# Performance work log

Measured on AMD Instinct MI355X. Metric: run time of the kernel, lower is better.

The kernel has to match this reference:

```python
import jax, jax.numpy as jnp
import numpy as np

COST_CLASS, COST_BBOX, COST_MASK = 1.0, 5.0, 2.0
EPS = 1e-6


def setup_inputs() -> dict:
    key = jax.random.key(0)
    k = jax.random.split(key, 8)
    B, Q, M, C1, H, W = 8, 300, 100, 81, 128, 128
    pred_logits = jax.random.normal(k[0], (B, Q, C1), jnp.float32)
    # boxes as valid xyxy in [0,1]: lo in [0,.5], size in [0,.5]
    plo = jax.random.uniform(k[1], (B, Q, 2)) * 0.5
    psz = jax.random.uniform(k[2], (B, Q, 2)) * 0.5
    pred_boxes = jnp.concatenate([plo, plo + psz], axis=-1)
    pred_masks = jax.random.normal(k[3], (B, Q, H, W), jnp.float32)
    gt_labels = jax.random.randint(k[4], (B, M), 0, C1, dtype=jnp.int32)
    glo = jax.random.uniform(k[5], (B, M, 2)) * 0.5
    gsz = jax.random.uniform(k[6], (B, M, 2)) * 0.5
    gt_boxes = jnp.concatenate([glo, glo + gsz], axis=-1)
    gt_masks = (jax.random.uniform(k[7], (B, M, H, W)) > 0.5).astype(jnp.float32)
    valid = jnp.ones((B, M), jnp.bool_)
    return dict(pred_logits=pred_logits, pred_boxes=pred_boxes, pred_masks=pred_masks,
                gt_labels=gt_labels, gt_boxes=gt_boxes, gt_masks=gt_masks, valid=valid)


def _giou(b1, b2):
    # b1 [Q,4], b2 [M,4] (xyxy) -> [Q,M] generalized IoU
    lt = jnp.maximum(b1[:, None, :2], b2[None, :, :2])
    rb = jnp.minimum(b1[:, None, 2:], b2[None, :, 2:])
    wh = jnp.clip(rb - lt, 0.0)
    inter = wh[..., 0] * wh[..., 1]
    a1 = (b1[:, 2] - b1[:, 0]) * (b1[:, 3] - b1[:, 1])
    a2 = (b2[:, 2] - b2[:, 0]) * (b2[:, 3] - b2[:, 1])
    union = a1[:, None] + a2[None, :] - inter
    iou = inter / (union + EPS)
    ltm = jnp.minimum(b1[:, None, :2], b2[None, :, :2])
    rbm = jnp.maximum(b1[:, None, 2:], b2[None, :, 2:])
    whm = jnp.clip(rbm - ltm, 0.0)
    am = whm[..., 0] * whm[..., 1]
    return iou - (am - union) / (am + EPS)


@jax.jit
def _cost_matrix(pred_logits, pred_boxes, pred_masks, gt_labels, gt_boxes, gt_masks):
    B, Q = pred_logits.shape[:2]
    M = gt_labels.shape[1]
    probs = jax.nn.softmax(pred_logits, axis=-1)                      # [B,Q,C+1]
    idx = jnp.broadcast_to(gt_labels[:, None, :].astype(jnp.int32), (B, Q, M))
    cost_class = -jnp.take_along_axis(probs, idx, axis=2)             # [B,Q,M]
    # L1 cdist
    cost_bbox = jnp.abs(pred_boxes[:, :, None, :] - gt_boxes[:, None, :, :]).sum(-1)
    cost_giou = -jax.vmap(_giou)(pred_boxes, gt_boxes)                # [B,Q,M]
    # dice cost
    pm = jax.nn.sigmoid(pred_masks).reshape(B, Q, -1)                 # [B,Q,HW]
    gm = gt_masks.reshape(B, M, -1).astype(pm.dtype)                  # [B,M,HW]
    num = 2.0 * jnp.einsum('bqc,bmc->bqm', pm, gm)
    den = pm.sum(-1)[:, :, None] + gm.sum(-1)[:, None, :]
    cost_mask = 1.0 - num / (den + EPS)
    # NOTE: faithful to source quirk -- giou term is folded into cost_bbox
    # and therefore weighted by COST_BBOX.
    return (COST_CLASS * cost_class + COST_BBOX * (cost_bbox + cost_giou)
            + COST_MASK * cost_mask)


def _hungarian(cost):
    # Jonker-Volgenant style shortest-augmenting-path assignment (e-maxx).
    # cost: np [n,m] with n <= m. Returns p[m]: row assigned to each col (-1 if none).
    n, m = cost.shape
    u = np.zeros(n)
    v = np.zeros(m)
    p = np.full(m, -1, np.int64)
    for i in range(n):
        minv = np.full(m, np.inf)
        way = np.full(m, -1, np.int64)
        used = np.zeros(m, bool)
        cur_row, j0 = i, -1
        while True:
            cur = cost[cur_row] - u[cur_row] - v
            upd = (~used) & (cur < minv)
            minv[upd] = cur[upd]
            way[upd] = j0
            mv = np.where(used, np.inf, minv)
            j1 = int(np.argmin(mv))
            delta = mv[j1]
            u[i] += delta
            uj = np.nonzero(used)[0]
            if uj.size:
                u[p[uj]] += delta
                v[uj] -= delta
            minv[~used] -= delta
            used[j1] = True
            j0 = j1
            cur_row = p[j1]
            if cur_row == -1:
                break
        j = j0
        while j != -1:
            jp = way[j]
            p[j] = p[jp] if jp != -1 else i
            j = jp
    return p


def reference(pred_logits, pred_boxes, pred_masks, gt_labels, gt_boxes, gt_masks, valid):
    # valid is all-ones (num_gt == max_objects for every sample), so the
    # per-sample variable-size slicing in the torch loop reduces to full M.
    C = _cost_matrix(pred_logits, pred_boxes, pred_masks, gt_labels, gt_boxes, gt_masks)
    Cn = np.asarray(C, dtype=np.float64)
    preds, gts = [], []
    for b in range(Cn.shape[0]):
        # solve on transpose: rows = gt (M=100) <= cols = queries (Q=300)
        p = _hungarian(Cn[b].T)            # p[q] = matched gt index or -1
        q = np.nonzero(p >= 0)[0]          # sorted pred indices (scipy convention)
        preds.append(q)
        gts.append(p[q])
    pred_idx = jnp.asarray(np.stack(preds), dtype=jnp.int32)  # [B, M]
    gt_idx = jnp.asarray(np.stack(gts), dtype=jnp.int32)      # [B, M]
    return C, pred_idx, gt_idx
```

## Files before the change

kernel.cpp:

```cpp
#include <hip/hip_runtime.h>

#define HW 16384
#define NQ 300
#define NM 100
#define NB 8
#define NC 81
#define KCH 1024
#define NKC 16
#define CTP 304

typedef __attribute__((ext_vector_type(8))) short frag8;
typedef __attribute__((ext_vector_type(4))) float float4v;
typedef __attribute__((ext_vector_type(4))) unsigned short ushort4v;

__device__ __forceinline__ unsigned short f2bf(float f) {
  union { float f; unsigned u; } c; c.f = f;
  unsigned r = c.u + 0x7FFFu + ((c.u >> 16) & 1u);
  return (unsigned short)(r >> 16);
}

__global__ __launch_bounds__(256) void prep_kernel(
    const float* __restrict__ pmask, const float* __restrict__ gmask,
    unsigned short* __restrict__ pm, unsigned short* __restrict__ gm,
    float* __restrict__ psum, float* __restrict__ gsum) {
  int row = blockIdx.x;
  int t = threadIdx.x;
  bool isP = row < NB * NQ;
  const float* srcf = isP ? (pmask + (size_t)row * HW)
                          : (gmask + (size_t)(row - NB * NQ) * HW);
  unsigned short* dst = isP ? (pm + (size_t)row * HW)
                            : (gm + (size_t)(row - NB * NQ) * HW);
  const float4v* src = (const float4v*)srcf;
  float s = 0.f;
  for (int i = t; i < HW / 4; i += 256) {
    float4v x = src[i];
    float y0, y1, y2, y3;
    if (isP) {
      y0 = 1.f / (1.f + __expf(-x.x));
      y1 = 1.f / (1.f + __expf(-x.y));
      y2 = 1.f / (1.f + __expf(-x.z));
      y3 = 1.f / (1.f + __expf(-x.w));
    } else { y0 = x.x; y1 = x.y; y2 = x.z; y3 = x.w; }
    s += (y0 + y1) + (y2 + y3);
    ushort4v o = { f2bf(y0), f2bf(y1), f2bf(y2), f2bf(y3) };
    *(ushort4v*)(dst + i * 4) = o;
  }
  for (int off = 32; off > 0; off >>= 1) s += __shfl_xor(s, off, 64);
  __shared__ float red[4];
  int wave = t >> 6, lane = t & 63;
  if (lane == 0) red[wave] = s;
  __syncthreads();
  if (t == 0) {
    float tot = (red[0] + red[1]) + (red[2] + red[3]);
    if (isP) psum[row] = tot; else gsum[row - NB * NQ] = tot;
  }
}

__global__ __launch_bounds__(256) void softmax_kernel(
    const float* __restrict__ logits, float* __restrict__ probs) {
  int wave = threadIdx.x >> 6, lane = threadIdx.x & 63;
  int row = blockIdx.x * 4 + wave;
  const float* in = logits + (size_t)row * NC;
  float x0 = (lane < NC) ? in[lane] : -1e30f;
  float x1 = (lane + 64 < NC) ? in[lane + 64] : -1e30f;
  float mx = fmaxf(x0, x1);
  for (int off = 32; off > 0; off >>= 1) mx = fmaxf(mx, __shfl_xor(mx, off, 64));
  float e0 = (lane < NC) ? __expf(x0 - mx) : 0.f;
  float e1 = (lane + 64 < NC) ? __expf(x1 - mx) : 0.f;
  float s = e0 + e1;
  for (int off = 32; off > 0; off >>= 1) s += __shfl_xor(s, off, 64);
  float inv = 1.f / s;
  if (lane < NC) probs[(size_t)row * NC + lane] = e0 * inv;
  if (lane + 64 < NC) probs[(size_t)row * NC + lane + 64] = e1 * inv;
}

__global__ __launch_bounds__(64) void dot_kernel(
    const unsigned short* __restrict__ pm, const unsigned short* __restrict__ gm,
    float* __restrict__ dotv) {
  int qt = blockIdx.x;
  int b = blockIdx.y >> 4, kc = blockIdx.y & 15;
  int lane = threadIdx.x;
  int q0 = qt * 16;
  int row_a = q0 + (lane & 15);
  int ra = (row_a < NQ) ? row_a : NQ - 1;
  int koff = (lane >> 4) * 8;
  const unsigned short* pA = pm + ((size_t)b * NQ + ra) * HW + kc * KCH + koff;
  const unsigned short* pB0 = gm + (size_t)b * NM * HW + kc * KCH + koff;
  const unsigned short* pB[7];
#pragma unroll
  for (int mt = 0; mt < 7; ++mt) {
    int row_b = mt * 16 + (lane & 15);
    int rb = (row_b < NM) ? row_b : NM - 1;
    pB[mt] = pB0 + (size_t)rb * HW;
  }
  float4v acc[7];
#pragma unroll
  for (int mt = 0; mt < 7; ++mt) acc[mt] = (float4v){0.f, 0.f, 0.f, 0.f};
#pragma unroll 2
  for (int k = 0; k < KCH; k += 32) {
    frag8 a = *(const frag8*)(pA + k);
#pragma unroll
    for (int mt = 0; mt < 7; ++mt) {
      frag8 bb = *(const frag8*)(pB[mt] + k);
      acc[mt] = __builtin_amdgcn_mfma_f32_16x16x32_bf16(a, bb, acc[mt], 0, 0, 0);
    }
  }
#pragma unroll
  for (int mt = 0; mt < 7; ++mt) {
    int cm = mt * 16 + (lane & 15);
    if (cm < NM) {
#pragma unroll
      for (int r = 0; r < 4; ++r) {
        int cq = q0 + (lane >> 4) * 4 + r;
        if (cq < NQ)
          unsafeAtomicAdd(&dotv[((size_t)b * NQ + cq) * NM + cm], acc[mt][r]);
      }
    }
  }
}

__global__ __launch_bounds__(256) void combine_kernel(
    const float* __restrict__ dotv, const float* __restrict__ psum,
    const float* __restrict__ gsum, const float* __restrict__ probs,
    const int* __restrict__ labels, const float* __restrict__ pboxes,
    const float* __restrict__ gboxes, float* __restrict__ outC,
    float* __restrict__ ct) {
  int idx = blockIdx.x * 256 + threadIdx.x;
  if (idx >= NB * NQ * NM) return;
  int b = idx / (NQ * NM);
  int r = idx - b * (NQ * NM);
  int q = r / NM;
  int m = r - q * NM;
  float num = 2.f * dotv[idx];
  float den = psum[b * NQ + q] + gsum[b * NM + m];
  float cmask = 1.f - num / (den + 1e-6f);
  int lab = labels[b * NM + m];
  float cclass = -probs[((size_t)b * NQ + q) * NC + lab];
  const float* pb = pboxes + ((size_t)b * NQ + q) * 4;
  const float* gb = gboxes + ((size_t)b * NM + m) * 4;
  float p0 = pb[0], p1 = pb[1], p2 = pb[2], p3 = pb[3];
  float g0 = gb[0], g1 = gb[1], g2 = gb[2], g3 = gb[3];
  float cbbox = fabsf(p0 - g0) + fabsf(p1 - g1) + fabsf(p2 - g2) + fabsf(p3 - g3);
  float iw = fmaxf(fminf(p2, g2) - fmaxf(p0, g0), 0.f);
  float ih = fmaxf(fminf(p3, g3) - fmaxf(p1, g1), 0.f);
  float inter = iw * ih;
  float a1 = (p2 - p0) * (p3 - p1), a2 = (g2 - g0) * (g3 - g1);
  float uni = a1 + a2 - inter;
  float iou = inter / (uni + 1e-6f);
  float aw = fmaxf(fmaxf(p2, g2) - fminf(p0, g0), 0.f);
  float ah = fmaxf(fmaxf(p3, g3) - fminf(p1, g1), 0.f);
  float am = aw * ah;
  float giou = iou - (am - uni) / (am + 1e-6f);
  float C = cclass + 5.f * (cbbox - giou) + 2.f * cmask;
  outC[idx] = C;
  ct[((size_t)b * NM + m) * CTP + q] = C;
}

extern __shared__ char hsmem[];
__global__ __launch_bounds__(64) void hungarian_kernel(
    const float* __restrict__ ct, float* __restrict__ out) {
  float* cost   = (float*)hsmem;
  float* u      = (float*)(hsmem + 121600);
  int*   p      = (int*)(hsmem + 122000);
  int*   way    = (int*)(hsmem + 123280);
  int*   colOwn = (int*)(hsmem + 124560);
  int*   rowUsed= (int*)(hsmem + 125840);
  int*   queue  = (int*)(hsmem + 126240);
  int*   qmisc  = (int*)(hsmem + 127840);
  const int b = blockIdx.x;
  const int lane = threadIdx.x;
  const float INF = __builtin_inff();

  {
    const float4v* a4 = (const float4v*)(ct + (size_t)b * NM * CTP);
    float4v* c4 = (float4v*)cost;
    for (int i = lane; i < NM * CTP / 4; i += 64) c4[i] = a4[i];
  }
#pragma unroll
  for (int w = 0; w < 5; ++w) {
    p[lane + 64 * w] = -1;
    colOwn[lane + 64 * w] = 0x7fffffff;
  }
  if (lane == 0) { qmisc[0] = 0; qmisc[1] = 0; }
  float v[5];
#pragma unroll
  for (int w = 0; w < 5; ++w) v[w] = 0.f;
  __syncthreads();

  int rarg0 = 0, rarg1 = 0;
  {
    int i = lane;
    float mv = INF; int cj = 0;
    for (int j = 0; j < NQ; ++j) {
      float c = cost[i * CTP + j];
      if (c < mv) { mv = c; cj = j; }
    }
    u[i] = mv; rarg0 = cj;
  }
  if (lane < NM - 64) {
    int i = lane + 64;
    float mv = INF; int cj = 0;
    for (int j = 0; j < NQ; ++j) {
      float c = cost[i * CTP + j];
      if (c < mv) { mv = c; cj = j; }
    }
    u[i] = mv; rarg1 = cj;
  }
  atomicMin(&colOwn[rarg0], lane);
  if (lane < NM - 64) atomicMin(&colOwn[rarg1], lane + 64);
  __syncthreads();
  int free0 = 0, free1 = 0;
  {
    bool won = (colOwn[rarg0] == lane);
    if (won) p[rarg0] = lane;
    rowUsed[lane] = won ? 1 : 0;
    free0 = won ? 0 : 1;
  }
  if (lane < NM - 64) {
    bool won = (colOwn[rarg1] == lane + 64);
    if (won) p[rarg1] = lane + 64;
    rowUsed[lane + 64] = won ? 1 : 0;
    free1 = won ? 0 : 1;
  }
  {
    unsigned long long m0 = __ballot(free0 != 0);
    if (free0) queue[__popcll(m0 & ((1ull << lane) - 1ull))] = lane;
    int base = (int)__popcll(m0);
    unsigned long long m1 = __ballot(free1 != 0);
    if (free1) queue[base + (int)__popcll(m1 & ((1ull << lane) - 1ull))] = lane + 64;
    base += (int)__popcll(m1);
    if (lane == 0) qmisc[1] = base;
  }

  int pops = 0;
  while (true) {
    __syncthreads();
    int h = qmisc[0], t = qmisc[1];
    if (h >= t || pops >= 192) break;
    int i = queue[h];
    ++pops;
    if (lane == 0) qmisc[0] = h + 1;
    float m1 = INF, m2 = INF; int jl = 0;
#pragma unroll
    for (int w = 0; w < 5; ++w) {
      int j = lane + 64 * w;
      float tt = (j < NQ) ? (cost[i * CTP + j] - v[w]) : INF;
      if (tt < m1) { m2 = m1; m1 = tt; jl = j; } else if (tt < m2) m2 = tt;
    }
    unsigned long long best;
    {
      unsigned sb = __float_as_uint(m1);
      sb = (sb >> 31) ? ~sb : (sb | 0x80000000u);
      best = ((unsigned long long)sb << 32) | (unsigned)jl;
    }
    for (int off = 32; off > 0; off >>= 1) {
      unsigned long long o = __shfl_xor(best, off, 64);
      if (o < best) best = o;
    }
    int j1 = (int)(best & 0xFFFFFFFFu);
    float m1g;
    {
      unsigned sb = (unsigned)(best >> 32);
      m1g = __uint_as_float((sb >> 31) ? (sb ^ 0x80000000u) : ~sb);
    }
    float c2 = (jl == j1) ? m2 : m1;
    for (int off = 32; off > 0; off >>= 1) c2 = fminf(c2, __shfl_xor(c2, off, 64));
    float delta = (c2 > m1g) ? (c2 - m1g) : 0.f;
    int i1 = p[j1];
    if (i1 >= 0 && delta <= 0.f) {
      if (lane == 0) u[i] = c2;
      continue;
    }
#pragma unroll
    for (int w = 0; w < 5; ++w) if (lane + 64 * w == j1) v[w] -= delta;
    if (lane == 0) {
      u[i] = c2;
      p[j1] = i;
      rowUsed[i] = 1;
      if (i1 >= 0) { rowUsed[i1] = 0; queue[t] = i1; qmisc[1] = t + 1; }
    }
  }
  __syncthreads();

  for (int i = 0; i < NM; ++i) {
    if (rowUsed[i]) continue;
    float dv[5]; int usedR[5];
#pragma unroll
    for (int w = 0; w < 5; ++w) {
      int j = lane + 64 * w;
      dv[w] = INF;
      usedR[w] = (j >= NQ) ? 1 : 0;
      way[j] = -1;
    }
    float S = 0.f;
    int nr = i, j0 = -1;
    while (true) {
      float urow = u[nr];
      unsigned long long best = ~0ull;
#pragma unroll
      for (int w = 0; w < 5; ++w) {
        if (!usedR[w]) {
          int j = lane + 64 * w;
          float cand = S + cost[nr * CTP + j] - urow - v[w];
          if (cand < dv[w]) { dv[w] = cand; way[j] = j0; }
          unsigned sb = __float_as_uint(dv[w]);
          sb = (sb >> 31) ? ~sb : (sb | 0x80000000u);
          unsigned long long key = ((unsigned long long)sb << 32) | (unsigned)j;
          if (key < best) best = key;
        }
      }
      for (int off = 32; off > 0; off >>= 1) {
        unsigned long long o = __shfl_xor(best, off, 64);
        if (o < best) best = o;
      }
      int j1 = (int)(best & 0xFFFFFFFFu);
      {
        unsigned sb = (unsigned)(best >> 32);
        S = __uint_as_float((sb >> 31) ? (sb ^ 0x80000000u) : ~sb);
      }
#pragma unroll
      for (int w = 0; w < 5; ++w) if (lane + 64 * w == j1) usedR[w] = 1;
      j0 = j1;
      int nr2 = p[j1];
      if (nr2 < 0) break;
      nr = nr2;
    }
#pragma unroll
    for (int w = 0; w < 5; ++w) {
      int j = lane + 64 * w;
      if (j < NQ && usedR[w]) {
        float amt = S - dv[w];
        v[w] -= amt;
        int pj = p[j];
        if (pj >= 0) u[pj] += amt;
      }
    }
    if (lane == 0) u[i] += S;
    __syncthreads();
    if (lane == 0) {
      int j = j0;
      while (j != -1) {
        int jp = way[j];
        p[j] = (jp != -1) ? p[jp] : i;
        j = jp;
      }
      rowUsed[i] = 1;
    }
    __syncthreads();
  }

  {
    float* po = out + NB * NQ * NM + b * NM;
    float* go = out + NB * NQ * NM + NB * NM + b * NM;
    int base = 0;
#pragma unroll
    for (int w = 0; w < 5; ++w) {
      int j = lane + 64 * w;
      int pj = (j < NQ) ? p[j] : -1;
      unsigned long long mask = __ballot(pj >= 0);
      if (pj >= 0) {
        int pos = base + (int)__popcll(mask & ((1ull << lane) - 1ull));
        po[pos] = (float)j;
        go[pos] = (float)pj;
      }
      base += (int)__popcll(mask);
    }
  }
}

extern "C" void kernel_launch(void* const* d_in, const int* in_sizes, int n_in,
                              void* d_out, int out_size, void* d_ws, size_t ws_size,
                              hipStream_t stream) {
  const float* logits = (const float*)d_in[0];
  const float* pboxes = (const float*)d_in[1];
  const float* pmask  = (const float*)d_in[2];
  const int*   labels = (const int*)d_in[3];
  const float* gboxes = (const float*)d_in[4];
  const float* gmask  = (const float*)d_in[5];
  float* out = (float*)d_out;
  char* ws = (char*)d_ws;

  unsigned short* pm   = (unsigned short*)(ws + 0);
  unsigned short* gmb  = (unsigned short*)(ws + 78643200);
  float* psum  = (float*)(ws + 104857600);
  float* gsum  = (float*)(ws + 104867200);
  float* probs = (float*)(ws + 104870400);
  float* dotv  = (float*)(ws + 105648000);
  float* ct    = (float*)(ws + 106608000);

  hipFuncSetAttribute(reinterpret_cast<const void*>(hungarian_kernel),
                      hipFuncAttributeMaxDynamicSharedMemorySize, 127872);

  hipMemsetAsync(dotv, 0, NB * NQ * NM * sizeof(float), stream);
  hipLaunchKernelGGL(prep_kernel, dim3(NB * NQ + NB * NM), dim3(256), 0, stream,
                     pmask, gmask, pm, gmb, psum, gsum);
  hipLaunchKernelGGL(softmax_kernel, dim3(600), dim3(256), 0, stream, logits, probs);
  hipLaunchKernelGGL(dot_kernel, dim3(19, NB * NKC), dim3(64), 0, stream, pm, gmb, dotv);
  hipLaunchKernelGGL(combine_kernel, dim3((NB * NQ * NM + 255) / 256), dim3(256), 0, stream,
                     dotv, psum, gsum, probs, labels, pboxes, gboxes, out, ct);
  hipLaunchKernelGGL(hungarian_kernel, dim3(NB), dim3(64), 127872, stream, ct, out);
}
```

Before: 524.6 us.

## Speed up Hungarian kernel with DPP reductions and register-cached p/u

```diff
diff --git a/kernel.cpp b/kernel.cpp
--- a/kernel.cpp
+++ b/kernel.cpp
@@ -156,6 +156,23 @@
   ct[((size_t)b * NM + m) * CTP + q] = C;
 }
 
+__device__ __forceinline__ float wave_fmin_bcast(float x) {
+  int t;
+  t = __builtin_amdgcn_update_dpp(__float_as_int(x), __float_as_int(x), 0x111, 0xf, 0xf, false);
+  x = fminf(x, __int_as_float(t));
+  t = __builtin_amdgcn_update_dpp(__float_as_int(x), __float_as_int(x), 0x112, 0xf, 0xf, false);
+  x = fminf(x, __int_as_float(t));
+  t = __builtin_amdgcn_update_dpp(__float_as_int(x), __float_as_int(x), 0x114, 0xf, 0xf, false);
+  x = fminf(x, __int_as_float(t));
+  t = __builtin_amdgcn_update_dpp(__float_as_int(x), __float_as_int(x), 0x118, 0xf, 0xf, false);
+  x = fminf(x, __int_as_float(t));
+  t = __builtin_amdgcn_update_dpp(__float_as_int(x), __float_as_int(x), 0x142, 0xf, 0xf, false);
+  x = fminf(x, __int_as_float(t));
+  t = __builtin_amdgcn_update_dpp(__float_as_int(x), __float_as_int(x), 0x143, 0xf, 0xf, false);
+  x = fminf(x, __int_as_float(t));
+  return __int_as_float(__builtin_amdgcn_readlane(__float_as_int(x), 63));
+}
+
 extern __shared__ char hsmem[];
 __global__ __launch_bounds__(64) void hungarian_kernel(
     const float* __restrict__ ct, float* __restrict__ out) {
@@ -167,6 +184,7 @@
   int*   rowUsed= (int*)(hsmem + 125840);
   int*   queue  = (int*)(hsmem + 126240);
   int*   qmisc  = (int*)(hsmem + 127840);
+  int*   flist  = colOwn;
   const int b = blockIdx.x;
   const int lane = threadIdx.x;
   const float INF = __builtin_inff();
@@ -240,31 +258,27 @@
     int i = queue[h];
     ++pops;
     if (lane == 0) qmisc[0] = h + 1;
-    float m1 = INF, m2 = INF; int jl = 0;
+    float tv[5];
+    float m1 = INF, m2 = INF;
 #pragma unroll
     for (int w = 0; w < 5; ++w) {
       int j = lane + 64 * w;
       float tt = (j < NQ) ? (cost[i * CTP + j] - v[w]) : INF;
-      if (tt < m1) { m2 = m1; m1 = tt; jl = j; } else if (tt < m2) m2 = tt;
-    }
-    unsigned long long best;
-    {
-      unsigned sb = __float_as_uint(m1);
-      sb = (sb >> 31) ? ~sb : (sb | 0x80000000u);
-      best = ((unsigned long long)sb << 32) | (unsigned)jl;
-    }
-    for (int off = 32; off > 0; off >>= 1) {
-      unsigned long long o = __shfl_xor(best, off, 64);
-      if (o < best) best = o;
-    }
-    int j1 = (int)(best & 0xFFFFFFFFu);
-    float m1g;
-    {
-      unsigned sb = (unsigned)(best >> 32);
-      m1g = __uint_as_float((sb >> 31) ? (sb ^ 0x80000000u) : ~sb);
-    }
-    float c2 = (jl == j1) ? m2 : m1;
-    for (int off = 32; off > 0; off >>= 1) c2 = fminf(c2, __shfl_xor(c2, off, 64));
+      tv[w] = tt;
+      if (tt < m1) { m2 = m1; m1 = tt; } else if (tt < m2) m2 = tt;
+    }
+    float m1g = wave_fmin_bcast(m1);
+    int j1 = -1;
+#pragma unroll
+    for (int w = 0; w < 5; ++w) {
+      unsigned long long mk = __ballot(tv[w] == m1g);
+      if (j1 < 0 && mk) j1 = (int)__builtin_ctzll(mk) + 64 * w;
+    }
+    float c2c = INF;
+#pragma unroll
+    for (int w = 0; w < 5; ++w)
+      if (lane + 64 * w != j1) c2c = fminf(c2c, tv[w]);
+    float c2 = wave_fmin_bcast(c2c);
     float delta = (c2 > m1g) ? (c2 - m1g) : 0.f;
     int i1 = p[j1];
     if (i1 >= 0 && delta <= 0.f) {
@@ -282,8 +296,28 @@
   }
   __syncthreads();
 
-  for (int i = 0; i < NM; ++i) {
-    if (rowUsed[i]) continue;
+  int nfree;
+  {
+    int r0 = rowUsed[lane];
+    int r1 = (lane < NM - 64) ? rowUsed[lane + 64] : 1;
+    unsigned long long m0 = __ballot(r0 == 0);
+    if (!r0) flist[__popcll(m0 & ((1ull << lane) - 1ull))] = lane;
+    int base = (int)__popcll(m0);
+    unsigned long long m1 = __ballot(r1 == 0);
+    if (!r1) flist[base + (int)__popcll(m1 & ((1ull << lane) - 1ull))] = lane + 64;
+    nfree = base + (int)__popcll(m1);
+  }
+  __syncthreads();
+
+  int pr0, pr1, pr2, pr3, pr4;
+  float ur0, ur1;
+  pr0 = p[lane]; pr1 = p[lane + 64]; pr2 = p[lane + 128];
+  pr3 = p[lane + 192]; pr4 = p[lane + 256];
+  ur0 = u[lane];
+  ur1 = (lane < NM - 64) ? u[lane + 64] : 0.f;
+
+  for (int fi = 0; fi < nfree; ++fi) {
+    int i = flist[fi];
     float dv[5]; int usedR[5];
 #pragma unroll
     for (int w = 0; w < 5; ++w) {
@@ -295,33 +329,49 @@
     float S = 0.f;
     int nr = i, j0 = -1;
     while (true) {
-      float urow = u[nr];
-      unsigned long long best = ~0ull;
+      float urow;
+      {
+        int bits = (nr < 64)
+            ? __builtin_amdgcn_readlane(__float_as_int(ur0), nr & 63)
+            : __builtin_amdgcn_readlane(__float_as_int(ur1), nr & 63);
+        urow = __int_as_float(bits);
+      }
+      int base = nr * CTP;
+      float c0 = cost[base + lane];
+      float c1 = cost[base + lane + 64];
+      float c2_ = cost[base + lane + 128];
+      float c3 = cost[base + lane + 192];
+      float c4 = cost[base + lane + 256];
+      float cr[5] = {c0, c1, c2_, c3, c4};
+      float cmin = INF;
 #pragma unroll
       for (int w = 0; w < 5; ++w) {
         if (!usedR[w]) {
-          int j = lane + 64 * w;
-          float cand = S + cost[nr * CTP + j] - urow - v[w];
-          if (cand < dv[w]) { dv[w] = cand; way[j] = j0; }
-          unsigned sb = __float_as_uint(dv[w]);
-          sb = (sb >> 31) ? ~sb : (sb | 0x80000000u);
-          unsigned long long key = ((unsigned long long)sb << 32) | (unsigned)j;
-          if (key < best) best = key;
+          float cand = S + cr[w] - urow - v[w];
+          if (cand < dv[w]) { dv[w] = cand; way[lane + 64 * w] = j0; }
+          cmin = fminf(cmin, dv[w]);
         }
       }
-      for (int off = 32; off > 0; off >>= 1) {
-        unsigned long long o = __shfl_xor(best, off, 64);
-        if (o < best) best = o;
-      }
-      int j1 = (int)(best & 0xFFFFFFFFu);
-      {
-        unsigned sb = (unsigned)(best >> 32);
-        S = __uint_as_float((sb >> 31) ? (sb ^ 0x80000000u) : ~sb);
-      }
+      float m = wave_fmin_bcast(cmin);
+      int j1 = -1;
+#pragma unroll
+      for (int w = 0; w < 5; ++w) {
+        unsigned long long mk = __ballot(!usedR[w] && dv[w] == m);
+        if (j1 < 0 && mk) j1 = (int)__builtin_ctzll(mk) + 64 * w;
+      }
+      S = m;
 #pragma unroll
       for (int w = 0; w < 5; ++w) if (lane + 64 * w == j1) usedR[w] = 1;
       j0 = j1;
-      int nr2 = p[j1];
+      int nr2;
+      {
+        int sl = j1 >> 6, ln = j1 & 63;
+        if (sl == 0)      nr2 = __builtin_amdgcn_readlane(pr0, ln);
+        else if (sl == 1) nr2 = __builtin_amdgcn_readlane(pr1, ln);
+        else if (sl == 2) nr2 = __builtin_amdgcn_readlane(pr2, ln);
+        else if (sl == 3) nr2 = __builtin_amdgcn_readlane(pr3, ln);
+        else              nr2 = __builtin_amdgcn_readlane(pr4, ln);
+      }
       if (nr2 < 0) break;
       nr = nr2;
     }
@@ -331,7 +381,8 @@
       if (j < NQ && usedR[w]) {
         float amt = S - dv[w];
         v[w] -= amt;
-        int pj = p[j];
+        int pj = (w == 0) ? pr0 : (w == 1) ? pr1 : (w == 2) ? pr2
+               : (w == 3) ? pr3 : pr4;
         if (pj >= 0) u[pj] += amt;
       }
     }
@@ -344,9 +395,12 @@
         p[j] = (jp != -1) ? p[jp] : i;
         j = jp;
       }
-      rowUsed[i] = 1;
     }
     __syncthreads();
+    pr0 = p[lane]; pr1 = p[lane + 64]; pr2 = p[lane + 128];
+    pr3 = p[lane + 192]; pr4 = p[lane + 256];
+    ur0 = u[lane];
+    ur1 = (lane < NM - 64) ? u[lane + 64] : 0.f;
   }
 
   {
```

Measured after the change: 494.7 us. 5.7% less time.
